# Optimization experiments

Hardware: AMD Instinct MI355X
Metric: run time of the kernel (lower is better)

Reference implementation:

```python
import jax, jax.numpy as jnp
import numpy as np

GRID_RES_SAMPLE = 0.08  # config.grid_resolution_sample
VOXEL_SIZE = 0.04       # scene voxel size encoded in transforms


def setup_inputs() -> dict:
    key = jax.random.key(0)
    ks = jax.random.split(key, 4)
    B, X = 4, 96
    G = 192            # == ceil(X * GRID_RES_SAMPLE / VOXEL_SIZE), matches dynamic size_voxel_grid
    N = 500_000        # sparse occupied voxels per scene
    NUM_ADD = 5000     # static stand-in for occ_grids.sum()+100 mask augmentations
    # scene voxel-grid transform: scale VOXEL_SIZE, translate -5m (same structure per scene)
    T = np.eye(4, dtype=np.float32)
    T[0, 0] = T[1, 1] = T[2, 2] = VOXEL_SIZE
    T[:3, 3] = -5.0
    transforms = np.tile(T, (B, 1, 1)).astype(np.float32)
    transforms_inv = np.stack([np.linalg.inv(t) for t in transforms]).astype(np.float32)
    # per-batch regular coordinate grids with random world offsets in [0,1)m
    offs = np.asarray(jax.random.uniform(ks[0], (B, 3), dtype=jnp.float32))
    ax = np.arange(X, dtype=np.float32) * GRID_RES_SAMPLE
    gx, gy, gz = np.meshgrid(ax, ax, ax, indexing='ij')
    base = np.stack([gx, gy, gz], axis=0)  # [3,X,X,X]
    coords = (base[None] + offs[:, :, None, None, None]).astype(np.float32)
    sparse = jax.random.randint(ks[1], (B, N, 3), 0, 400, dtype=jnp.int32)
    rand_idx = jax.random.randint(ks[2], (3, NUM_ADD), 0, X, dtype=jnp.int32)
    conv_w = jnp.ones((1, 1, 5, 5, 5), jnp.float32)  # Conv3d(1,1,5) all-ones, no bias
    return {
        'coordinate_grids': jnp.asarray(coords),
        'transforms': jnp.asarray(transforms),
        'transforms_inv': jnp.asarray(transforms_inv),
        'sparse_encoding': sparse,
        'conv_w': conv_w,
        'rand_idx': rand_idx,
        'grid_size': G,
    }


def reference(coordinate_grids, transforms, transforms_inv, sparse_encoding, conv_w, rand_idx, grid_size):
    B, C, X, Y, Z = coordinate_grids.shape
    flat = coordinate_grids.reshape(B, 3, -1)
    min_loc = flat.min(-1)   # [B,3]
    max_loc = flat.max(-1)   # [B,3]
    max_size_grid = (max_loc + GRID_RES_SAMPLE - min_loc).max(0)  # [3]
    min_homo = jnp.concatenate([min_loc, jnp.ones((B, 1), flat.dtype)], axis=1)
    min_voxel_idx = jnp.floor(jnp.einsum('bij,bj->bi', transforms_inv, min_homo)[:, :3])
    min_voxel_idx = jnp.maximum(min_voxel_idx, 0.0)  # [B,3]
    size_vox = jnp.ceil(jnp.einsum('bij,j->bi', transforms_inv[:, :3, :3], max_size_grid).max(0))  # [3], == grid_size
    # shift sparse indices into the local window and filter out-of-range ones
    se = sparse_encoding.astype(jnp.float32) - min_voxel_idx[:, None, :]   # [B,N,3]
    valid = ((se >= 0) & (se < size_vox)).all(-1)                          # [B,N]
    sei = jnp.clip(se.astype(jnp.int32), 0, grid_size - 1)
    occ = jnp.zeros((B, grid_size, grid_size, grid_size), jnp.float32)
    b_idx = jnp.broadcast_to(jnp.arange(B)[:, None], valid.shape)
    occ = occ.at[b_idx, sei[..., 0], sei[..., 1], sei[..., 2]].max(valid.astype(jnp.float32))
    # world position of voxel (0,0,0) of the local window and window extent
    min_homo_idx = jnp.concatenate([min_voxel_idx, jnp.ones((B, 1), flat.dtype)], axis=1)
    pos_base = jnp.einsum('bij,bj->bi', transforms, min_homo_idx)[:, :3]   # [B,3]
    extent = jnp.einsum('bij,j->bi', transforms[:, :3, :3], size_vox)      # [B,3]
    voxel_size = extent / size_vox                                          # [B,3]
    # trilinear interpolation of dense occ grid at the coordinate grid (voxel-center convention)
    p = (coordinate_grids - pos_base[:, :, None, None, None]) / voxel_size[:, :, None, None, None] - 0.5
    p0 = jnp.floor(p)
    f = p - p0                       # [B,3,X,Y,Z]
    p0 = p0.astype(jnp.int32)
    bb = jnp.arange(B)[:, None, None, None]
    out = jnp.zeros((B, X, Y, Z), jnp.float32)
    for dx in (0, 1):
        for dy in (0, 1):
            for dz in (0, 1):
                ix = jnp.clip(p0[:, 0] + dx, 0, grid_size - 1)
                iy = jnp.clip(p0[:, 1] + dy, 0, grid_size - 1)
                iz = jnp.clip(p0[:, 2] + dz, 0, grid_size - 1)
                w = ((f[:, 0] if dx else 1 - f[:, 0]) *
                     (f[:, 1] if dy else 1 - f[:, 1]) *
                     (f[:, 2] if dz else 1 - f[:, 2]))
                out = out + w * occ[bb, ix, iy, iz]
    occ_grids = out[:, None]  # [B,1,X,Y,Z]
    # 5x5x5 all-ones conv mask
    conv = jax.lax.conv_general_dilated(
        occ_grids, conv_w, window_strides=(1, 1, 1),
        padding=[(2, 2), (2, 2), (2, 2)],
        dimension_numbers=('NCDHW', 'OIDHW', 'NCDHW'))
    mask = conv > 0
    # random-index mask augmentation (num_voxels_to_add fixed statically)
    num_add = rand_idx.shape[1]
    badd = jnp.arange(num_add) % B
    mask = mask.at[badd, 0, rand_idx[0], rand_idx[1], rand_idx[2]].set(True)
    return occ_grids.astype(bool), mask
```

## Files before the change

kernel.cpp:

```cpp
#include <hip/hip_runtime.h>
#include <math.h>

#define GS   192
#define XS   96
#define XS3  (XS*XS*XS)
#define GRS  0.08f

#define PI_OFF     256
#define PF_OFF     (256 + 1152*4)
#define OCC_OFF    16384
#define OCC_WORDS  (4*GS*GS*(GS/32))
#define OUTB_WORDS (4*XS*XS*(XS/32))
#define RAND_OFF   (OCC_OFF + OCC_WORDS*4)
#define OUT_OFF    (RAND_OFF + OUTB_WORDS*4)

__device__ __forceinline__ int clampi(int v, int lo, int hi) {
    return v < lo ? lo : (v > hi ? hi : v);
}

__global__ void k_scalars(const float* __restrict__ coords,
                          const float* __restrict__ T,
                          const float* __restrict__ Tinv,
                          float* ws,
                          const int* __restrict__ rand_idx,
                          unsigned* __restrict__ randb,
                          int B, int nadd) {
    __shared__ int imn[12], imx[12];
    __shared__ float SS[64];
    int t = threadIdx.x;
    for (int idx = t; idx < nadd; idx += 256) {
        int b = idx % B;
        int r0 = rand_idx[idx], r1 = rand_idx[nadd + idx], r2 = rand_idx[2*nadd + idx];
        int e = ((b*XS + r0)*XS + r1)*XS + r2;
        atomicOr(&randb[e >> 5], 1u << (e & 31));
    }
    if (t < 12) { imn[t] = 0x7F800000; imx[t] = 0; }
    __syncthreads();
    int tot = B * 3 * XS;
    for (int e = t; e < tot; e += 256) {
        int b = e / (3 * XS); int c = (e / XS) % 3; int i = e % XS;
        size_t off = (size_t)(b*3 + c) * XS3
                   + (c == 0 ? (size_t)i * XS * XS : (c == 1 ? (size_t)i * XS : (size_t)i));
        int v = __float_as_int(coords[off]);
        atomicMin(&imn[b*3 + c], v);
        atomicMax(&imx[b*3 + c], v);
    }
    __syncthreads();
    if (t == 0) {
        float mnl[12], mxl[12];
        for (int k = 0; k < 12; k++) { mnl[k] = __int_as_float(imn[k]); mxl[k] = __int_as_float(imx[k]); }
        float msg[3];
        for (int c = 0; c < 3; c++) {
            float m = -__builtin_inff();
            for (int b = 0; b < B; b++) {
                float v = __fadd_rn(mxl[b*3 + c], GRS);
                v = __fsub_rn(v, mnl[b*3 + c]);
                m = fmaxf(m, v);
            }
            msg[c] = m;
        }
        for (int b = 0; b < B; b++)
            for (int i = 0; i < 3; i++) {
                const float* R = Tinv + b*16 + i*4;
                float v = __fmul_rn(R[0], mnl[b*3 + 0]);
                v = __fadd_rn(v, __fmul_rn(R[1], mnl[b*3 + 1]));
                v = __fadd_rn(v, __fmul_rn(R[2], mnl[b*3 + 2]));
                v = __fadd_rn(v, R[3]);
                SS[24 + b*3 + i] = fmaxf(floorf(v), 0.0f);
            }
        for (int i = 0; i < 3; i++) {
            float m = -__builtin_inff();
            for (int b = 0; b < B; b++) {
                const float* R = Tinv + b*16 + i*4;
                float v = __fmul_rn(R[0], msg[0]);
                v = __fadd_rn(v, __fmul_rn(R[1], msg[1]));
                v = __fadd_rn(v, __fmul_rn(R[2], msg[2]));
                m = fmaxf(m, v);
            }
            SS[36 + i] = ceilf(m);
        }
        for (int b = 0; b < B; b++)
            for (int i = 0; i < 3; i++) {
                const float* R = T + b*16 + i*4;
                float v = __fmul_rn(R[0], SS[24 + b*3 + 0]);
                v = __fadd_rn(v, __fmul_rn(R[1], SS[24 + b*3 + 1]));
                v = __fadd_rn(v, __fmul_rn(R[2], SS[24 + b*3 + 2]));
                v = __fadd_rn(v, R[3]);
                SS[40 + b*3 + i] = v;
            }
        for (int b = 0; b < B; b++)
            for (int i = 0; i < 3; i++) {
                const float* R = T + b*16 + i*4;
                float v = __fmul_rn(R[0], SS[36 + 0]);
                v = __fadd_rn(v, __fmul_rn(R[1], SS[36 + 1]));
                v = __fadd_rn(v, __fmul_rn(R[2], SS[36 + 2]));
                SS[52 + b*3 + i] = v / SS[36 + i];
            }
        for (int k = 24; k < 64; k++) ws[k] = SS[k];
    }
    __syncthreads();
    int* PI = (int*)((char*)ws + PI_OFF);
    float* PF = (float*)((char*)ws + PF_OFF);
    for (int e = t; e < tot; e += 256) {
        int b = e / (3 * XS); int c = (e / XS) % 3; int i = e % XS;
        size_t off = (size_t)(b*3 + c) * XS3
                   + (c == 0 ? (size_t)i * XS * XS : (c == 1 ? (size_t)i * XS : (size_t)i));
        float v = coords[off];
        float p = (v - SS[40 + b*3 + c]) / SS[52 + b*3 + c] - 0.5f;
        float p0 = floorf(p);
        PI[e] = (int)p0;
        PF[e] = p - p0;
    }
}

__global__ void k_scatter(const int* __restrict__ sparse, const float* __restrict__ ws,
                          unsigned* __restrict__ occ, int N, int total) {
    int t = blockIdx.x * blockDim.x + threadIdx.x;
    if (t >= total) return;
    int b = t / N;
    const float* S = ws;
    int s0 = sparse[(size_t)t*3 + 0];
    int s1 = sparse[(size_t)t*3 + 1];
    int s2 = sparse[(size_t)t*3 + 2];
    float e0 = (float)s0 - S[24 + b*3 + 0];
    float e1 = (float)s1 - S[24 + b*3 + 1];
    float e2 = (float)s2 - S[24 + b*3 + 2];
    if (e0 >= 0.f && e0 < S[36+0] && e1 >= 0.f && e1 < S[36+1] && e2 >= 0.f && e2 < S[36+2]) {
        int x = clampi((int)e0, 0, GS-1);
        int y = clampi((int)e1, 0, GS-1);
        int z = clampi((int)e2, 0, GS-1);
        atomicOr(&occ[(((size_t)b*GS + x)*GS + y)*(GS/32) + (z >> 5)], 1u << (z & 31));
    }
}

__global__ __launch_bounds__(256) void k_interp(const float* __restrict__ ws,
                                                const unsigned* __restrict__ occ,
                                                int* __restrict__ out0,
                                                unsigned* __restrict__ outb,
                                                int total) {
    int gid = blockIdx.x * 256 + threadIdx.x;
    if (gid >= total) return;
    int z = gid % XS;
    int r1 = gid / XS;
    int y = r1 % XS;
    int r2 = r1 / XS;
    int x = r2 % XS;
    int b = r2 / XS;
    const int* PI = (const int*)((const char*)ws + PI_OFF);
    const float* PF = (const float*)((const char*)ws + PF_OFF);
    int ix = PI[(b*3 + 0)*XS + x]; float fx = PF[(b*3 + 0)*XS + x];
    int iy = PI[(b*3 + 1)*XS + y]; float fy = PF[(b*3 + 1)*XS + y];
    int iz = PI[(b*3 + 2)*XS + z]; float fz = PF[(b*3 + 2)*XS + z];
    int x0 = clampi(ix,   0, GS-1), x1 = clampi(ix+1, 0, GS-1);
    int y0 = clampi(iy,   0, GS-1), y1 = clampi(iy+1, 0, GS-1);
    int z0 = clampi(iz,   0, GS-1), z1 = clampi(iz+1, 0, GS-1);
    float wx0 = 1.f - fx, wx1 = fx, wy0 = 1.f - fy, wy1 = fy, wz0 = 1.f - fz, wz1 = fz;
    const unsigned* r00 = occ + (((size_t)b*GS + x0)*GS + y0)*(GS/32);
    const unsigned* r01 = occ + (((size_t)b*GS + x0)*GS + y1)*(GS/32);
    const unsigned* r10 = occ + (((size_t)b*GS + x1)*GS + y0)*(GS/32);
    const unsigned* r11 = occ + (((size_t)b*GS + x1)*GS + y1)*(GS/32);
    float w00 = wx0*wy0, w01 = wx0*wy1, w10 = wx1*wy0, w11 = wx1*wy1;
    float s = 0.f;
    s += w00*wz0*(float)((r00[z0>>5] >> (z0&31)) & 1u);
    s += w00*wz1*(float)((r00[z1>>5] >> (z1&31)) & 1u);
    s += w01*wz0*(float)((r01[z0>>5] >> (z0&31)) & 1u);
    s += w01*wz1*(float)((r01[z1>>5] >> (z1&31)) & 1u);
    s += w10*wz0*(float)((r10[z0>>5] >> (z0&31)) & 1u);
    s += w10*wz1*(float)((r10[z1>>5] >> (z1&31)) & 1u);
    s += w11*wz0*(float)((r11[z0>>5] >> (z0&31)) & 1u);
    s += w11*wz1*(float)((r11[z1>>5] >> (z1&31)) & 1u);
    bool nz = (s != 0.f);
    __builtin_nontemporal_store(nz ? 1 : 0, &out0[gid]);
    unsigned long long m = __ballot(nz);
    int lane = threadIdx.x & 63;
    if (lane == 0)  outb[gid >> 5] = (unsigned)m;
    if (lane == 32) outb[gid >> 5] = (unsigned)(m >> 32);
}

__global__ __launch_bounds__(256) void k_dilate_bits(const unsigned* __restrict__ outb,
                                                     unsigned* __restrict__ outb2,
                                                     int totalW) {
    int t = blockIdx.x * 256 + threadIdx.x;
    if (t >= totalW) return;
    int w = t % 3;
    int r1 = t / 3;
    int j = r1 % XS;
    int r2 = r1 / XS;
    int i = r2 % XS;
    int b = r2 / XS;
    unsigned accP = 0, accC = 0, accN = 0;
    for (int di = -2; di <= 2; di++) {
        int ii = i + di; if (ii < 0 || ii >= XS) continue;
        for (int dj = -2; dj <= 2; dj++) {
            int jj = j + dj; if (jj < 0 || jj >= XS) continue;
            const unsigned* row = outb + ((size_t)(b*XS + ii)*XS + jj)*3;
            accC |= row[w];
            if (w > 0) accP |= row[w-1];
            if (w < 2) accN |= row[w+1];
        }
    }
    unsigned d = accC
               | (accC << 1) | (accP >> 31)
               | (accC << 2) | (accP >> 30)
               | (accC >> 1) | (accN << 31)
               | (accC >> 2) | (accN << 30);
    outb2[t] = d;
}

__global__ __launch_bounds__(256) void k_expand(const unsigned* __restrict__ outb2,
                                                const unsigned* __restrict__ randb,
                                                int* __restrict__ out1, int total) {
    int gid = blockIdx.x * 256 + threadIdx.x;
    if (gid >= total) return;
    unsigned w = outb2[gid >> 5] | randb[gid >> 5];
    __builtin_nontemporal_store((int)((w >> (gid & 31)) & 1u), &out1[gid]);
}

extern "C" void kernel_launch(void* const* d_in, const int* in_sizes, int n_in,
                              void* d_out, int out_size, void* d_ws, size_t ws_size,
                              hipStream_t stream) {
    const float* coords = (const float*)d_in[0];
    const float* T      = (const float*)d_in[1];
    const float* Tinv   = (const float*)d_in[2];
    const int*   sparse = (const int*)d_in[3];
    const int*   rand_i = (const int*)d_in[5];
    int* out = (int*)d_out;

    int B = in_sizes[1] / 16;
    int N = in_sizes[3] / (B * 3);
    int nadd = in_sizes[5] / 3;

    float*    ws    = (float*)d_ws;
    unsigned* occ   = (unsigned*)((char*)d_ws + OCC_OFF);
    unsigned* randb = (unsigned*)((char*)d_ws + RAND_OFF);
    unsigned* outb  = (unsigned*)((char*)d_ws + OUT_OFF);
    unsigned* outb2 = occ;
    size_t half = (size_t)B * XS3;

    hipMemsetAsync((char*)d_ws + OCC_OFF, 0, (size_t)(OCC_WORDS + OUTB_WORDS) * 4, stream);

    k_scalars<<<1, 256, 0, stream>>>(coords, T, Tinv, ws, rand_i, randb, B, nadd);
    int totalPts = B * N;
    k_scatter<<<(totalPts + 255) / 256, 256, 0, stream>>>(sparse, ws, occ, N, totalPts);
    int total = B * XS3;
    k_interp<<<(total + 255) / 256, 256, 0, stream>>>(ws, occ, out, outb, total);
    int totalW = B * XS * XS * 3;
    k_dilate_bits<<<totalW / 256, 256, 0, stream>>>(outb, outb2, totalW);
    k_expand<<<(total + 255) / 256, 256, 0, stream>>>(outb2, randb, out + half, total);
}
```

Measured before the change: 162.3 us.

## Vectorize scatter loads, defer occ output to a combined bit-expand kernel

The scatter kernel now loads four points per thread as three int4 vectors, which cuts per-thread overhead and gives wider loads. k_interp no longer writes the full int occupancy output and only emits packed bits. A single final kernel expands both the occupancy bits and the dilated-mask bits into the two int outputs. The random-index bits are folded into the dilate kernel, and k_scalars runs with 1024 threads. This assumes B*N is divisible by 4 and that no group of four points crosses a batch boundary, and the dense writes lose their nontemporal hint.

```diff
diff --git a/kernel.cpp b/kernel.cpp
--- a/kernel.cpp
+++ b/kernel.cpp
@@ -18,17 +18,18 @@
     return v < lo ? lo : (v > hi ? hi : v);
 }
 
-__global__ void k_scalars(const float* __restrict__ coords,
-                          const float* __restrict__ T,
-                          const float* __restrict__ Tinv,
-                          float* ws,
-                          const int* __restrict__ rand_idx,
-                          unsigned* __restrict__ randb,
-                          int B, int nadd) {
+__global__ __launch_bounds__(1024) void k_scalars(
+        const float* __restrict__ coords,
+        const float* __restrict__ T,
+        const float* __restrict__ Tinv,
+        float* ws,
+        const int* __restrict__ rand_idx,
+        unsigned* __restrict__ randb,
+        int B, int nadd) {
     __shared__ int imn[12], imx[12];
     __shared__ float SS[64];
     int t = threadIdx.x;
-    for (int idx = t; idx < nadd; idx += 256) {
+    for (int idx = t; idx < nadd; idx += 1024) {
         int b = idx % B;
         int r0 = rand_idx[idx], r1 = rand_idx[nadd + idx], r2 = rand_idx[2*nadd + idx];
         int e = ((b*XS + r0)*XS + r1)*XS + r2;
@@ -37,7 +38,7 @@
     if (t < 12) { imn[t] = 0x7F800000; imx[t] = 0; }
     __syncthreads();
     int tot = B * 3 * XS;
-    for (int e = t; e < tot; e += 256) {
+    for (int e = t; e < tot; e += 1024) {
         int b = e / (3 * XS); int c = (e / XS) % 3; int i = e % XS;
         size_t off = (size_t)(b*3 + c) * XS3
                    + (c == 0 ? (size_t)i * XS * XS : (c == 1 ? (size_t)i * XS : (size_t)i));
@@ -101,7 +102,7 @@
     __syncthreads();
     int* PI = (int*)((char*)ws + PI_OFF);
     float* PF = (float*)((char*)ws + PF_OFF);
-    for (int e = t; e < tot; e += 256) {
+    for (int e = t; e < tot; e += 1024) {
         int b = e / (3 * XS); int c = (e / XS) % 3; int i = e % XS;
         size_t off = (size_t)(b*3 + c) * XS3
                    + (c == 0 ? (size_t)i * XS * XS : (c == 1 ? (size_t)i * XS : (size_t)i));
@@ -113,29 +114,35 @@
     }
 }
 
-__global__ void k_scatter(const int* __restrict__ sparse, const float* __restrict__ ws,
-                          unsigned* __restrict__ occ, int N, int total) {
-    int t = blockIdx.x * blockDim.x + threadIdx.x;
-    if (t >= total) return;
-    int b = t / N;
+__global__ __launch_bounds__(256) void k_scatter(const int4* __restrict__ sparse4,
+                                                 const float* __restrict__ ws,
+                                                 unsigned* __restrict__ occ,
+                                                 int N, int ngroups) {
+    int t = blockIdx.x * 256 + threadIdx.x;
+    if (t >= ngroups) return;
     const float* S = ws;
-    int s0 = sparse[(size_t)t*3 + 0];
-    int s1 = sparse[(size_t)t*3 + 1];
-    int s2 = sparse[(size_t)t*3 + 2];
-    float e0 = (float)s0 - S[24 + b*3 + 0];
-    float e1 = (float)s1 - S[24 + b*3 + 1];
-    float e2 = (float)s2 - S[24 + b*3 + 2];
-    if (e0 >= 0.f && e0 < S[36+0] && e1 >= 0.f && e1 < S[36+1] && e2 >= 0.f && e2 < S[36+2]) {
-        int x = clampi((int)e0, 0, GS-1);
-        int y = clampi((int)e1, 0, GS-1);
-        int z = clampi((int)e2, 0, GS-1);
-        atomicOr(&occ[(((size_t)b*GS + x)*GS + y)*(GS/32) + (z >> 5)], 1u << (z & 31));
+    int4 a = sparse4[3*t], b4 = sparse4[3*t + 1], c4 = sparse4[3*t + 2];
+    int pt[4][3] = { {a.x, a.y, a.z}, {a.w, b4.x, b4.y},
+                     {b4.z, b4.w, c4.x}, {c4.y, c4.z, c4.w} };
+    int b = (4*t) / N;
+    float m0 = S[24 + b*3 + 0], m1 = S[24 + b*3 + 1], m2 = S[24 + b*3 + 2];
+    float v0 = S[36 + 0], v1 = S[36 + 1], v2 = S[36 + 2];
+    #pragma unroll
+    for (int k = 0; k < 4; k++) {
+        float e0 = (float)pt[k][0] - m0;
+        float e1 = (float)pt[k][1] - m1;
+        float e2 = (float)pt[k][2] - m2;
+        if (e0 >= 0.f && e0 < v0 && e1 >= 0.f && e1 < v1 && e2 >= 0.f && e2 < v2) {
+            int x = clampi((int)e0, 0, GS-1);
+            int y = clampi((int)e1, 0, GS-1);
+            int z = clampi((int)e2, 0, GS-1);
+            atomicOr(&occ[(((size_t)b*GS + x)*GS + y)*(GS/32) + (z >> 5)], 1u << (z & 31));
+        }
     }
 }
 
 __global__ __launch_bounds__(256) void k_interp(const float* __restrict__ ws,
                                                 const unsigned* __restrict__ occ,
-                                                int* __restrict__ out0,
                                                 unsigned* __restrict__ outb,
                                                 int total) {
     int gid = blockIdx.x * 256 + threadIdx.x;
@@ -170,7 +177,6 @@
     s += w11*wz0*(float)((r11[z0>>5] >> (z0&31)) & 1u);
     s += w11*wz1*(float)((r11[z1>>5] >> (z1&31)) & 1u);
     bool nz = (s != 0.f);
-    __builtin_nontemporal_store(nz ? 1 : 0, &out0[gid]);
     unsigned long long m = __ballot(nz);
     int lane = threadIdx.x & 63;
     if (lane == 0)  outb[gid >> 5] = (unsigned)m;
@@ -178,6 +184,7 @@
 }
 
 __global__ __launch_bounds__(256) void k_dilate_bits(const unsigned* __restrict__ outb,
+                                                     const unsigned* __restrict__ randb,
                                                      unsigned* __restrict__ outb2,
                                                      int totalW) {
     int t = blockIdx.x * 256 + threadIdx.x;
@@ -204,16 +211,18 @@
                | (accC << 2) | (accP >> 30)
                | (accC >> 1) | (accN << 31)
                | (accC >> 2) | (accN << 30);
-    outb2[t] = d;
-}
-
-__global__ __launch_bounds__(256) void k_expand(const unsigned* __restrict__ outb2,
-                                                const unsigned* __restrict__ randb,
-                                                int* __restrict__ out1, int total) {
+    outb2[t] = d | randb[t];
+}
+
+__global__ __launch_bounds__(256) void k_expand2(const unsigned* __restrict__ outb,
+                                                 const unsigned* __restrict__ outb2,
+                                                 int* __restrict__ out0,
+                                                 int* __restrict__ out1, int total) {
     int gid = blockIdx.x * 256 + threadIdx.x;
     if (gid >= total) return;
-    unsigned w = outb2[gid >> 5] | randb[gid >> 5];
-    __builtin_nontemporal_store((int)((w >> (gid & 31)) & 1u), &out1[gid]);
+    int word = gid >> 5, bit = gid & 31;
+    out0[gid] = (int)((outb[word]  >> bit) & 1u);
+    out1[gid] = (int)((outb2[word] >> bit) & 1u);
 }
 
 extern "C" void kernel_launch(void* const* d_in, const int* in_sizes, int n_in,
@@ -239,12 +248,12 @@
 
     hipMemsetAsync((char*)d_ws + OCC_OFF, 0, (size_t)(OCC_WORDS + OUTB_WORDS) * 4, stream);
 
-    k_scalars<<<1, 256, 0, stream>>>(coords, T, Tinv, ws, rand_i, randb, B, nadd);
-    int totalPts = B * N;
-    k_scatter<<<(totalPts + 255) / 256, 256, 0, stream>>>(sparse, ws, occ, N, totalPts);
+    k_scalars<<<1, 1024, 0, stream>>>(coords, T, Tinv, ws, rand_i, randb, B, nadd);
+    int ngroups = B * N / 4;
+    k_scatter<<<(ngroups + 255) / 256, 256, 0, stream>>>((const int4*)sparse, ws, occ, N, ngroups);
     int total = B * XS3;
-    k_interp<<<(total + 255) / 256, 256, 0, stream>>>(ws, occ, out, outb, total);
+    k_interp<<<(total + 255) / 256, 256, 0, stream>>>(ws, occ, outb, total);
     int totalW = B * XS * XS * 3;
-    k_dilate_bits<<<totalW / 256, 256, 0, stream>>>(outb, outb2, totalW);
-    k_expand<<<(total + 255) / 256, 256, 0, stream>>>(outb2, randb, out + half, total);
-}
+    k_dilate_bits<<<totalW / 256, 256, 0, stream>>>(outb, randb, outb2, totalW);
+    k_expand2<<<(total + 255) / 256, 256, 0, stream>>>(outb, outb2, out, out + half, total);
+}
```

Result: no change. 162.3 us (-0.0%).
